# Kernel tuning notes

Measured on AMD Instinct MI355X. Metric: run time of the kernel, lower is better.

The kernel has to match this reference:

```python
import jax, jax.numpy as jnp
import numpy as np
from functools import partial

# FCOSPostProcessor config (from __init__ defaults / hard-coded forward constants)
PRE_NMS_THRESH = 0.05
PRE_NMS_TOP_N = 1000
ML_NMS_THRESH = 0.6       # self.nms_thresh used in select_over_all_levels
FPN_POST_NMS_TOP_N = 100
SCORE_THRESH = 0.5        # hard-coded in forward
FINAL_NMS_THRESH = 0.9    # hard-coded in forward
NUM_CLASSES = 17          # 16 foreground logit channels

_STRIDES = (8, 16, 32, 64, 128)
_FEAT_HW = ((100, 160), (50, 80), (25, 40), (13, 20), (7, 10))
_BATCH = 8
_C = NUM_CLASSES - 1


def setup_inputs() -> dict:
    key = jax.random.key(0)
    inp = {}
    for lvl, (s, (h, w)) in enumerate(zip(_STRIDES, _FEAT_HW)):
        k1, k2, k3 = jax.random.split(jax.random.fold_in(key, lvl), 3)
        ys = jnp.arange(h, dtype=jnp.float32) * s + s // 2
        xs = jnp.arange(w, dtype=jnp.float32) * s + s // 2
        yy, xx = jnp.meshgrid(ys, xs, indexing='ij')
        inp[f'locations_{lvl}'] = jnp.stack([xx.reshape(-1), yy.reshape(-1)], axis=-1)  # (h*w, 2) xy
        inp[f'box_cls_{lvl}'] = jax.random.normal(k1, (_BATCH, _C, h, w), jnp.float32) * 2.0 - 5.0
        inp[f'box_regression_{lvl}'] = jax.random.uniform(k2, (_BATCH, 4, h, w), jnp.float32) * (4.0 * s)
        inp[f'centerness_{lvl}'] = jax.random.normal(k3, (_BATCH, 1, h, w), jnp.float32)
    inp['image_sizes'] = jnp.tile(jnp.array([[800, 1280]], jnp.int32), (_BATCH, 1))  # (h, w)
    return inp


def _decode_level(loc, cls, reg, ctr, image_sizes):
    # cls: (N,C,H,W) -> (N,HW,C) sigmoid; reg: (N,4,H,W) -> (N,HW,4); ctr: (N,1,H,W) -> (N,HW)
    N, C, H, W = cls.shape
    cls_s = jax.nn.sigmoid(jnp.transpose(cls, (0, 2, 3, 1)).reshape(N, H * W, C))
    reg_r = jnp.transpose(reg, (0, 2, 3, 1)).reshape(N, H * W, 4)
    ctr_s = jax.nn.sigmoid(ctr.reshape(N, H * W))
    cand = (cls_s > PRE_NMS_THRESH).reshape(N, -1)          # candidate mask (N, HW*C)
    sc = (cls_s * ctr_s[:, :, None]).reshape(N, -1)         # cls * centerness
    masked = jnp.where(cand, sc, -1.0)
    top_s, top_i = jax.lax.top_k(masked, PRE_NMS_TOP_N)     # padded top-k over threshold survivors
    valid = jnp.take_along_axis(cand, top_i, axis=1)
    loc_i = top_i // C
    labels = (top_i % C + 1).astype(jnp.int32)              # per_class = idx + 1
    pl = loc[loc_i]                                         # (N,K,2)
    idx4 = jnp.broadcast_to(loc_i[:, :, None], loc_i.shape + (4,))
    pr = jnp.take_along_axis(reg_r, idx4, axis=1)           # (N,K,4)
    x1 = pl[..., 0] - pr[..., 0]
    y1 = pl[..., 1] - pr[..., 1]
    x2 = pl[..., 0] + pr[..., 2]
    y2 = pl[..., 1] + pr[..., 3]
    # clip_to_image (TO_REMOVE = 1)
    hmax = (image_sizes[:, 0] - 1).astype(x1.dtype)[:, None]
    wmax = (image_sizes[:, 1] - 1).astype(x1.dtype)[:, None]
    boxes = jnp.stack([jnp.clip(x1, 0.0, wmax), jnp.clip(y1, 0.0, hmax),
                       jnp.clip(x2, 0.0, wmax), jnp.clip(y2, 0.0, hmax)], axis=-1)
    scores = jnp.where(valid, jnp.sqrt(jnp.maximum(top_s, 1e-12)), 0.0)  # sqrt(cls*ctr)
    return boxes, scores, labels, valid


def _iou(a, b):
    area_a = jnp.maximum(a[:, 2] - a[:, 0], 0.0) * jnp.maximum(a[:, 3] - a[:, 1], 0.0)
    area_b = jnp.maximum(b[:, 2] - b[:, 0], 0.0) * jnp.maximum(b[:, 3] - b[:, 1], 0.0)
    lt = jnp.maximum(a[:, None, :2], b[None, :, :2])
    rb = jnp.minimum(a[:, None, 2:], b[None, :, 2:])
    wh = jnp.maximum(rb - lt, 0.0)
    inter = wh[..., 0] * wh[..., 1]
    return inter / jnp.maximum(area_a[:, None] + area_b[None, :] - inter, 1e-9)


def _greedy_keep(boxes, scores, valid, thresh):
    # fixed-size greedy NMS on a single image; selection is discrete -> stop_gradient
    boxes = jax.lax.stop_gradient(boxes)
    scores = jax.lax.stop_gradient(scores)
    K = scores.shape[0]
    order = jnp.argsort(-jnp.where(valid, scores, -1.0))
    b = boxes[order]
    v = valid[order]
    iou = _iou(b, b)
    idx = jnp.arange(K)
    def body(i, keep):
        sup = (iou[i] > thresh) & keep[i] & (idx > i)
        return keep & (~sup)
    keep = jax.lax.fori_loop(0, K, body, v)
    return jnp.zeros(K, bool).at[order].set(keep)


def _pipeline(locs, clss, regs, ctrs, image_sizes):
    parts = [_decode_level(l, c, r, t, image_sizes)
             for l, c, r, t in zip(locs, clss, regs, ctrs)]
    boxes = jnp.concatenate([p[0] for p in parts], axis=1)   # (N, 5K, 4)
    scores = jnp.concatenate([p[1] for p in parts], axis=1)
    labels = jnp.concatenate([p[2] for p in parts], axis=1)
    valid = jnp.concatenate([p[3] for p in parts], axis=1)
    # multi-class NMS (boxlist_ml_nms): offset boxes per class so classes never overlap
    off = labels.astype(boxes.dtype) * (jax.lax.stop_gradient(jnp.max(boxes)) + 1.0)
    keep = jax.vmap(partial(_greedy_keep, thresh=ML_NMS_THRESH))(boxes + off[..., None], scores, valid)
    valid = valid & keep
    # fpn_post_nms_top_n cap (kthvalue-threshold in torch ~= top-k by score)
    _, idx = jax.lax.top_k(jnp.where(valid, scores, -1.0), FPN_POST_NMS_TOP_N)
    boxes = jnp.take_along_axis(boxes, jnp.broadcast_to(idx[:, :, None], idx.shape + (4,)), axis=1)
    scores = jnp.take_along_axis(scores, idx, axis=1)
    labels = jnp.take_along_axis(labels, idx, axis=1)
    valid = jnp.take_along_axis(valid, idx, axis=1)
    # choose_confident_boxes(score_thresh=0.5)
    valid = valid & (scores > SCORE_THRESH)
    # final class-agnostic boxlist_nms(0.9)
    keep2 = jax.vmap(partial(_greedy_keep, thresh=FINAL_NMS_THRESH))(boxes, scores, valid)
    valid = valid & keep2
    return (jnp.where(valid[..., None], boxes, 0.0),
            jnp.where(valid, scores, 0.0),
            jnp.where(valid, labels, 0),
            valid)


def reference(locations_0, locations_1, locations_2, locations_3, locations_4,
              box_cls_0, box_cls_1, box_cls_2, box_cls_3, box_cls_4,
              box_regression_0, box_regression_1, box_regression_2, box_regression_3, box_regression_4,
              centerness_0, centerness_1, centerness_2, centerness_3, centerness_4,
              image_sizes):
    locs = (locations_0, locations_1, locations_2, locations_3, locations_4)
    clss = (box_cls_0, box_cls_1, box_cls_2, box_cls_3, box_cls_4)
    regs = (box_regression_0, box_regression_1, box_regression_2, box_regression_3, box_regression_4)
    ctrs = (centerness_0, centerness_1, centerness_2, centerness_3, centerness_4)
    return _pipeline(locs, clss, regs, ctrs, image_sizes)
```

## Files before the change

kernel.cpp:

```cpp
#include <hip/hip_runtime.h>

#pragma clang fp contract(off)

typedef unsigned int u32;
typedef unsigned long long u64;
typedef unsigned char u8;

#define NIMG 8
#define NCLS 16
#define KSEL 1000
#define KIMG 5000
#define TOPN 100
#define CAP 576
#define NWRD 9
#define TIECAP 128
#define EPI 341280
#define HCH 4096
#define HBLK 84
#define ECH 16384
#define EBLK 23

__device__ inline int lvl_of(int i) {
  return (i < 256000) ? 0 : (i < 320000) ? 1 : (i < 336000) ? 2 : (i < 340160) ? 3 : 4;
}
__device__ inline int c_hw(int l)   { return l==0?16000: l==1?4000: l==2?1000: l==3?260: 70; }
__device__ inline int c_eoff(int l) { return l==0?0: l==1?256000: l==2?320000: l==3?336000: l==4?340160: 341280; }
__device__ inline int c_e(int l)    { return l==0?256000: l==1?64000: l==2?16000: l==3?4160: 1120; }

__device__ inline void blk_map(int b, int& lvl, int& bb, int& start, int& end) {
  if (b < 16)      { lvl = 0; bb = b; }
  else if (b < 20) { lvl = 1; bb = b - 16; }
  else             { lvl = b - 18; bb = 0; }
  start = c_eoff(lvl) + bb*ECH;
  int e = c_eoff(lvl + 1);
  end = (start + ECH < e) ? (start + ECH) : e;
}

struct Ptrs {
  const float* loc[5];
  const float* cls[5];
  const float* reg[5];
  const float* ctr[5];
  const int*   imsz;
};

__device__ inline u64 lmask_lt(int lane) { return lane ? (~0ull >> (64 - lane)) : 0ull; }

__device__ inline float sigm(float x) { return 1.0f / (1.0f + expf(-x)); }

__device__ inline float score_cand(const Ptrs& P, int img, int lvl, int c, int hw, bool& cand) {
  int HW = c_hw(lvl);
  float s = sigm(P.cls[lvl][(img*NCLS + c)*HW + hw]);
  cand = s > 0.05f;
  float t = sigm(P.ctr[lvl][img*HW + hw]);
  return s * t;
}

__device__ inline void box_decode(const Ptrs& P, int img, int lvl, int hw,
                                  float& x1, float& y1, float& x2, float& y2) {
  int HW = c_hw(lvl);
  float px = P.loc[lvl][hw*2+0];
  float py = P.loc[lvl][hw*2+1];
  float rl = P.reg[lvl][(img*4+0)*HW + hw];
  float rt = P.reg[lvl][(img*4+1)*HW + hw];
  float rr = P.reg[lvl][(img*4+2)*HW + hw];
  float rb = P.reg[lvl][(img*4+3)*HW + hw];
  float wmax = (float)(P.imsz[img*2+1] - 1);
  float hmax = (float)(P.imsz[img*2+0] - 1);
  x1 = fminf(fmaxf(px - rl, 0.0f), wmax);
  y1 = fminf(fmaxf(py - rt, 0.0f), hmax);
  x2 = fminf(fmaxf(px + rr, 0.0f), wmax);
  y2 = fminf(fmaxf(py + rb, 0.0f), hmax);
}

struct Det { float x1, y1, x2, y2, raw; bool cand; };

__device__ inline Det decode(const Ptrs& P, int img, int lvl, int c, int hw) {
  Det d;
  d.raw = score_cand(P, img, lvl, c, hw, d.cand);
  box_decode(P, img, lvl, hw, d.x1, d.y1, d.x2, d.y2);
  return d;
}

__device__ inline float iou_ref(float ax1, float ay1, float ax2, float ay2,
                                float bx1, float by1, float bx2, float by2) {
  float areaA = fmaxf(ax2-ax1, 0.0f) * fmaxf(ay2-ay1, 0.0f);
  float areaB = fmaxf(bx2-bx1, 0.0f) * fmaxf(by2-by1, 0.0f);
  float wx = fmaxf(fminf(ax2,bx2) - fmaxf(ax1,bx1), 0.0f);
  float wy = fmaxf(fminf(ay2,by2) - fmaxf(ay1,by1), 0.0f);
  float inter = wx * wy;
  return inter / fmaxf(areaA + areaB - inter, 1e-9f);
}

__global__ void k_zero(u32* w, int n) {
  for (int i = blockIdx.x*blockDim.x + threadIdx.x; i < n; i += gridDim.x*blockDim.x) {
    u32 val = 0;
    int rel = i - 40960;
    if (rel >= 0 && rel < 320 && (rel & 7) == 2) val = KSEL;
    w[i] = val;
  }
}

__global__ __launch_bounds__(256) void k_hist(Ptrs P, u32* hist, const u32* state, int pass) {
  __shared__ u32 lh[2][1024];
  int img = blockIdx.y;
  int chunk = blockIdx.x * HCH;
  for (int b = threadIdx.x; b < 2048; b += 256) ((u32*)lh)[b] = 0;
  int lvl0 = lvl_of(chunk);
  int prob0 = img*5 + lvl0;
  bool straddle = (lvl0 < 4) && (chunk + HCH > c_eoff(lvl0+1));
  u32 m0 = state[prob0*8+0], p0 = state[prob0*8+1];
  u32 m1 = 0, p1 = 0;
  if (straddle) { m1 = state[(prob0+1)*8+0]; p1 = state[(prob0+1)*8+1]; }
  int shift = (pass == 0) ? 20 : ((pass == 1) ? 10 : 0);
  __syncthreads();
  for (int k = 0; k < 16; ++k) {
    int i = chunk + k*256 + threadIdx.x;
    if (i >= EPI) break;
    int lvl = lvl0 + ((straddle && i >= c_eoff(lvl0+1)) ? 1 : 0);
    int li = i - c_eoff(lvl);
    int HW = c_hw(lvl);
    int c = li / HW, hw = li - c*HW;
    bool cand; float raw = score_cand(P, img, lvl, c, hw, cand);
    if (!cand) continue;
    u32 bits = __float_as_uint(raw);
    int bank = lvl - lvl0;
    u32 msk = bank ? m1 : m0, pfx = bank ? p1 : p0;
    if ((bits & msk) != pfx) continue;
    atomicAdd(&lh[bank][(bits >> shift) & 0x3FFu], 1u);
  }
  __syncthreads();
  for (int b = threadIdx.x; b < 2048; b += 256) {
    u32 v = ((u32*)lh)[b];
    if (v) atomicAdd(&hist[(prob0 + (b >> 10))*1024 + (b & 1023)], v);
  }
}

__global__ __launch_bounds__(256) void k_scan(u32* hist, u32* state, int pass) {
  __shared__ u32 sfx[1024];
  __shared__ int sbin;
  int prob = blockIdx.x;
  u32* h = hist + prob*1024;
  int tid = threadIdx.x;
  for (int r = tid; r < 1024; r += 256) sfx[r] = h[1023 - r];
  __syncthreads();
  for (int b = tid; b < 1024; b += 256) h[b] = 0;
  if (tid == 0) sbin = -1;
  for (int d = 1; d < 1024; d <<= 1) {
    u32 v[4];
#pragma unroll
    for (int k = 0; k < 4; ++k) {
      int i = tid + k*256;
      v[k] = sfx[i] + ((i >= d) ? sfx[i - d] : 0u);
    }
    __syncthreads();
#pragma unroll
    for (int k = 0; k < 4; ++k) sfx[tid + k*256] = v[k];
    __syncthreads();
  }
  u32 need = state[prob*8+2];
  u32 allM = state[prob*8+3];
  if (!allM) {
#pragma unroll
    for (int k = 0; k < 4; ++k) {
      int b = tid + k*256;
      u32 sb  = sfx[1023 - b];
      u32 sb1 = (b == 1023) ? 0u : sfx[1022 - b];
      if (sb >= need && sb1 < need) sbin = b;
    }
  }
  __syncthreads();
  if (tid == 0 && !allM) {
    u32* st = state + prob*8;
    if (sbin < 0) {
      st[3] = 1; st[0] = 0xFFFFFFFFu; st[1] = 0xFFFFFFFFu;
    } else {
      int shift = (pass == 0) ? 20 : ((pass == 1) ? 10 : 0);
      u32 rem = need - ((sbin == 1023) ? 0u : sfx[1022 - sbin]);
      st[1] |= ((u32)sbin) << shift;
      st[0] |= 0x3FFu << shift;
      st[2] = rem;
      if (pass == 2) { st[4] = st[1]; st[5] = rem; }
    }
  }
}

__global__ __launch_bounds__(256) void k_count(Ptrs P, const u32* state, u32* blockCnt) {
  int lvl, bb, start, end;
  blk_map(blockIdx.x, lvl, bb, start, end);
  int img = blockIdx.y;
  int prob = img*5 + lvl;
  int HW = c_hw(lvl);
  const float* clsBase = P.cls[lvl] + (size_t)img*NCLS*HW;
  const float* ctrBase = P.ctr[lvl] + (size_t)img*HW;
  u32 allMode = state[prob*8+3];
  u32 tstar = state[prob*8+4];
  int cnt = 0;
  for (int r = 0; r < 16; ++r) {
    int i0 = start + r*1024 + threadIdx.x*4;
    if (i0 >= end) continue;
    int li = i0 - c_eoff(lvl);
    float4 cv;
    if (i0 + 4 <= end) cv = *reinterpret_cast<const float4*>(clsBase + li);
    else {
      cv.x = clsBase[li];
      cv.y = (i0+1 < end) ? clsBase[li+1] : 0.0f;
      cv.z = (i0+2 < end) ? clsBase[li+2] : 0.0f;
      cv.w = (i0+3 < end) ? clsBase[li+3] : 0.0f;
    }
#pragma unroll
    for (int e = 0; e < 4; ++e) {
      int i = i0 + e;
      if (i >= end) break;
      float s = sigm((&cv.x)[e]);
      if (!(s > 0.05f)) continue;
      int lie = li + e;
      int hw = lie % HW;
      float t = sigm(ctrBase[hw]);
      u32 bits = __float_as_uint(s * t);
      if (allMode || bits > tstar) ++cnt;
    }
  }
  for (int d = 32; d >= 1; d >>= 1) cnt += __shfl_xor(cnt, d);
  __shared__ int ws[4];
  if ((threadIdx.x & 63) == 0) ws[threadIdx.x >> 6] = cnt;
  __syncthreads();
  if (threadIdx.x == 0) blockCnt[prob*16 + bb] = (u32)(ws[0] + ws[1] + ws[2] + ws[3]);
}

__global__ void k_bscan(const u32* blockCnt, u32* bbase, u32* counter) {
  int p = threadIdx.x;
  if (p >= 40) return;
  int lvl = p % 5;
  int nb = (lvl == 0) ? 16 : (lvl == 1) ? 4 : 1;
  u32 run = 0;
  for (int b = 0; b < nb; ++b) { bbase[p*16 + b] = run; run += blockCnt[p*16 + b]; }
  counter[p] = run;
}

__global__ __launch_bounds__(256) void k_emit(Ptrs P, const u32* state, const u32* bbase,
                                              u32* tieCnt, u32* tieIdx,
                                              u32* sbits, float* ssqrt, u32* slabel,
                                              float* sbox, u32* gmax) {
  __shared__ u32 wcnt[2][4];
  int lvl, bb, start, end;
  blk_map(blockIdx.x, lvl, bb, start, end);
  int img = blockIdx.y;
  int prob = img*5 + lvl;
  int HW = c_hw(lvl);
  const float* clsBase = P.cls[lvl] + (size_t)img*NCLS*HW;
  const float* ctrBase = P.ctr[lvl] + (size_t)img*HW;
  u32 allMode = state[prob*8+3];
  u32 tstar = state[prob*8+4];
  int lane = threadIdx.x & 63, wv = threadIdx.x >> 6;
  u64 lt = lmask_lt(lane);
  int running = (int)bbase[prob*16 + bb];
  float wmax = 0.0f;
  for (int r = 0; r < 16; ++r) {
    int i0 = start + r*1024 + threadIdx.x*4;
    int li = i0 - c_eoff(lvl);
    bool w[4] = {false,false,false,false};
    u32 bits[4] = {0,0,0,0};
    if (i0 < end) {
      float4 cv;
      if (i0 + 4 <= end) cv = *reinterpret_cast<const float4*>(clsBase + li);
      else {
        cv.x = clsBase[li];
        cv.y = (i0+1 < end) ? clsBase[li+1] : 0.0f;
        cv.z = (i0+2 < end) ? clsBase[li+2] : 0.0f;
        cv.w = (i0+3 < end) ? clsBase[li+3] : 0.0f;
      }
#pragma unroll
      for (int e = 0; e < 4; ++e) {
        int i = i0 + e;
        if (i >= end) break;
        float s = sigm((&cv.x)[e]);
        if (!(s > 0.05f)) continue;
        int lie = li + e;
        int c = lie / HW, hw = lie - c*HW;
        float t = sigm(ctrBase[hw]);
        u32 bi = __float_as_uint(s * t);
        if (allMode || bi > tstar) { w[e] = true; bits[e] = bi; }
        else if (bi == tstar) {
          u32 ts = atomicAdd(&tieCnt[prob], 1u);
          if (ts < TIECAP) tieIdx[prob*TIECAP + ts] = (u32)(hw*NCLS + c);
        }
      }
    }
    u64 b0 = __ballot(w[0]), b1 = __ballot(w[1]), b2 = __ballot(w[2]), b3 = __ballot(w[3]);
    int wvTot = (int)(__popcll(b0) + __popcll(b1) + __popcll(b2) + __popcll(b3));
    if (lane == 0) wcnt[r & 1][wv] = (u32)wvTot;
    __syncthreads();
    int preWave = 0, blockTot = 0;
#pragma unroll
    for (int k = 0; k < 4; ++k) {
      int v = (int)wcnt[r & 1][k];
      if (k < wv) preWave += v;
      blockTot += v;
    }
    int before = (int)(__popcll(b0 & lt) + __popcll(b1 & lt) + __popcll(b2 & lt) + __popcll(b3 & lt));
    int myBase = running + preWave + before;
    int acc = 0;
#pragma unroll
    for (int e = 0; e < 4; ++e) {
      if (!w[e]) continue;
      int slot = myBase + acc; ++acc;
      if (slot < KSEL) {
        int lie = li + e;
        int c = lie / HW, hw = lie - c*HW;
        float raw = __uint_as_float(bits[e]);
        float x1, y1, x2, y2;
        box_decode(P, img, lvl, hw, x1, y1, x2, y2);
        int idx = img*KIMG + lvl*KSEL + slot;
        sbits[idx]  = bits[e];
        ssqrt[idx]  = sqrtf(fmaxf(raw, 1e-12f));
        slabel[idx] = (u32)(c + 1);
        sbox[idx*4+0] = x1; sbox[idx*4+1] = y1;
        sbox[idx*4+2] = x2; sbox[idx*4+3] = y2;
        wmax = fmaxf(wmax, fmaxf(fmaxf(x1, y1), fmaxf(x2, y2)));
      }
    }
    running += blockTot;
  }
  for (int d = 32; d >= 1; d >>= 1) wmax = fmaxf(wmax, __shfl_xor(wmax, d));
  if (lane == 0 && wmax > 0.0f) atomicMax(gmax, __float_as_uint(wmax));
}

__global__ void k_ties(Ptrs P, const u32* state, u32* counter, const u32* tieCnt, const u32* tieIdx,
                       u32* sbits, float* ssqrt, u32* slabel, float* sbox, u32* gmax) {
  __shared__ u32 a[TIECAP];
  int prob = blockIdx.x;
  const u32* st = state + prob*8;
  if (st[3]) return;
  if (threadIdx.x != 0) return;
  int tn = (tieCnt[prob] < (u32)TIECAP) ? (int)tieCnt[prob] : TIECAP;
  int need = (int)st[5];
  int take = need < tn ? need : tn;
  if (take <= 0) return;
  for (int k = 0; k < tn; ++k) a[k] = tieIdx[prob*TIECAP + k];
  for (int k = 1; k < tn; ++k) {
    u32 v = a[k]; int m = k - 1;
    while (m >= 0 && a[m] > v) { a[m+1] = a[m]; --m; }
    a[m+1] = v;
  }
  int img = prob/5, lvl = prob%5;
  u32 cnt = counter[prob];
  for (int k = 0; k < take && cnt < (u32)KSEL; ++k) {
    u32 e = a[k]; int hw = (int)(e >> 4), c = (int)(e & 15u);
    Det d = decode(P, img, lvl, c, hw);
    int idx = img*KIMG + lvl*KSEL + (int)cnt;
    sbits[idx]  = __float_as_uint(d.raw);
    ssqrt[idx]  = sqrtf(fmaxf(d.raw, 1e-12f));
    slabel[idx] = (u32)(c + 1);
    sbox[idx*4+0] = d.x1; sbox[idx*4+1] = d.y1;
    sbox[idx*4+2] = d.x2; sbox[idx*4+3] = d.y2;
    float m4 = fmaxf(fmaxf(d.x1, d.y1), fmaxf(d.x2, d.y2));
    atomicMax(gmax, __float_as_uint(m4));
    ++cnt;
  }
  counter[prob] = cnt;
}

__global__ void k_deficit(Ptrs P, const u32* counter, u32* gmax) {
  int prob = blockIdx.x;
  int cnt = (int)counter[prob];
  if (cnt >= KSEL) return;
  int deficit = KSEL - cnt;
  int img = prob/5, lvl = prob%5;
  int E = c_e(lvl);
  int HW = c_hw(lvl);
  const float* clsBase = P.cls[lvl] + (size_t)img*NCLS*HW;
  int lane = threadIdx.x;
  int found = 0;
  float wmax = 0.0f;
  for (int base = 0; base < E && found < deficit; base += 64) {
    int e = base + lane;
    bool nc = false;
    if (e < E) nc = !(sigm(clsBase[(e & 15)*HW + (e >> 4)]) > 0.05f);
    u64 m = __ballot(nc);
    int pos = found + (int)__popcll(m & lmask_lt(lane));
    if (nc && pos < deficit) {
      float x1, y1, x2, y2;
      box_decode(P, img, lvl, e >> 4, x1, y1, x2, y2);
      wmax = fmaxf(wmax, fmaxf(fmaxf(x1, y1), fmaxf(x2, y2)));
    }
    found += (int)__popcll(m);
  }
  for (int d = 32; d >= 1; d >>= 1) wmax = fmaxf(wmax, __shfl_xor(wmax, d));
  if (lane == 0 && wmax > 0.0f) atomicMax(gmax, __float_as_uint(wmax));
}

__global__ __launch_bounds__(1024) void k_sort(const u32* sbits, u64* skey) {
  __shared__ u64 sk[8192];
  int img = blockIdx.x;
  int tid = threadIdx.x, nth = blockDim.x;
  for (int i = tid; i < 8192; i += nth)
    sk[i] = (i < KIMG) ? ((((u64)sbits[img*KIMG + i]) << 32) | (u32)(KIMG - 1 - i)) : 0ull;
  __syncthreads();
  for (int ksz = 2; ksz <= 8192; ksz <<= 1) {
    for (int j = ksz >> 1; j >= 1; j >>= 1) {
      for (int i = tid; i < 8192; i += nth) {
        int ixj = i ^ j;
        if (ixj > i) {
          bool desc = ((i & ksz) == 0);
          u64 a = sk[i], b = sk[ixj];
          if (desc ? (a < b) : (a > b)) { sk[i] = b; sk[ixj] = a; }
        }
      }
      __syncthreads();
    }
  }
  for (int i = tid; i < KIMG; i += nth) skey[img*KIMG + i] = sk[i];
}

__device__ inline int key_slot(u64 key) { return KIMG - 1 - (int)(key & 0xFFFFFFFFu); }

__global__ __launch_bounds__(256) void k_nms(const u64* skey, const u32* slabel, const float* sbox,
                                             const u32* gmax, u8* keep) {
  __shared__ float4 sb[CAP];
  __shared__ u32 srank[CAP];
  __shared__ u64 bm[CAP][NWRD];
  __shared__ u32 wcnt[4];
  __shared__ u64 kw[NWRD];
  __shared__ int sn;
  int img = blockIdx.x >> 4;
  int cls = (blockIdx.x & 15) + 1;
  int tid = threadIdx.x;
  int lane = tid & 63;
  int wv = tid >> 6;
  float off = (float)cls * (__uint_as_float(*gmax) + 1.0f);
  if (tid == 0) sn = 0;
  __syncthreads();
  for (int base = 0; base < KIMG; base += 256) {
    int r = base + tid;
    bool v = false; int slot = 0;
    if (r < KIMG) {
      u64 key = skey[img*KIMG + r];
      slot = key_slot(key);
      if ((key >> 32) != 0) v = (slabel[img*KIMG + slot] == (u32)cls);
    }
    u64 m = __ballot(v);
    int wrank = (int)__popcll(m & lmask_lt(lane));
    if (lane == 0) wcnt[wv] = (u32)__popcll(m);
    __syncthreads();
    int pos = sn + wrank;
    for (int k = 0; k < 4; ++k) if (k < wv) pos += (int)wcnt[k];
    if (v && pos < CAP) {
      const float* b = &sbox[(img*KIMG + slot)*4];
      sb[pos] = make_float4(b[0]+off, b[1]+off, b[2]+off, b[3]+off);
      srank[pos] = (u32)r;
    }
    __syncthreads();
    if (tid == 0) sn += (int)(wcnt[0]+wcnt[1]+wcnt[2]+wcnt[3]);
    __syncthreads();
  }
  int n = sn; if (n > CAP) n = CAP;
  for (int i = tid; i < n; i += 256) {
    float4 bi = sb[i];
    u64 w[NWRD];
#pragma unroll
    for (int q = 0; q < NWRD; ++q) w[q] = 0;
    for (int j = i + 1; j < n; ++j) {
      float4 bj = sb[j];
      if (iou_ref(bj.x,bj.y,bj.z,bj.w, bi.x,bi.y,bi.z,bi.w) > 0.6f)
        w[j >> 6] |= (1ull << (j & 63));
    }
#pragma unroll
    for (int q = 0; q < NWRD; ++q) bm[i][q] = w[q];
  }
  __syncthreads();
  if (wv == 0) {
    u64 kp = 0;
    if (lane < NWRD) {
      int cnt = n - lane*64;
      kp = (cnt >= 64) ? ~0ull : (cnt > 0 ? ((1ull << cnt) - 1ull) : 0ull);
    }
    for (int i = 0; i < n; ++i) {
      u64 row = (lane < NWRD) ? bm[i][lane] : 0ull;
      u64 kow = __shfl(kp, i >> 6);
      if ((kow >> (i & 63)) & 1ull) kp &= ~row;
    }
    if (lane < NWRD) kw[lane] = kp;
  }
  __syncthreads();
  for (int j = tid; j < n; j += 256)
    keep[img*KIMG + (int)srank[j]] = (u8)((kw[j >> 6] >> (j & 63)) & 1ull);
}

__global__ __launch_bounds__(64) void k_final(const u64* skey, const u8* keep, const float* ssqrt,
                                              const u32* slabel, const float* sbox, float* out) {
  __shared__ float sc[TOPN];
  __shared__ u32 lb[TOPN];
  __shared__ float4 bx[TOPN];
  int img = blockIdx.x;
  int lane = threadIdx.x;
  int cnt = 0;
  for (int base = 0; base < KIMG && cnt < TOPN; base += 64) {
    int r = base + lane;
    bool v = false; int slot = 0;
    if (r < KIMG) {
      u64 key = skey[img*KIMG + r];
      slot = key_slot(key);
      v = ((key >> 32) != 0) && (keep[img*KIMG + r] != 0);
    }
    u64 m = __ballot(v);
    int pos = cnt + (int)__popcll(m & lmask_lt(lane));
    if (v && pos < TOPN) {
      int sidx = img*KIMG + slot;
      sc[pos] = ssqrt[sidx];
      lb[pos] = slabel[sidx];
      bx[pos] = make_float4(sbox[sidx*4+0], sbox[sidx*4+1], sbox[sidx*4+2], sbox[sidx*4+3]);
    }
    cnt += (int)__popcll(m);
  }
  int n2 = cnt < TOPN ? cnt : TOPN;
  __syncthreads();
  u32 sup = 0;
  for (int i = 0; i < n2; ++i) {
    int owner = i & 63, s = i >> 6;
    u32 om = __shfl(sup, owner);
    bool vi = sc[i] > 0.5f;
    if (!vi || ((om >> s) & 1u)) continue;
    float4 bi = bx[i];
#pragma unroll
    for (int k = 0; k < 2; ++k) {
      int j = lane + (k << 6);
      if (j > i && j < n2 && !((sup >> k) & 1u)) {
        float4 bj = bx[j];
        if (iou_ref(bj.x, bj.y, bj.z, bj.w, bi.x, bi.y, bi.z, bi.w) > 0.9f)
          sup |= (1u << k);
      }
    }
  }
#pragma unroll
  for (int k = 0; k < 2; ++k) {
    int j = lane + (k << 6);
    if (j < TOPN) {
      bool ok = (j < n2) && (sc[j] > 0.5f) && !((sup >> k) & 1u);
      float4 b = ok ? bx[j] : make_float4(0.f, 0.f, 0.f, 0.f);
      float s  = ok ? sc[j] : 0.0f;
      float lf = ok ? (float)lb[j] : 0.0f;
      float vf = ok ? 1.0f : 0.0f;
      int ob = img*TOPN + j;
      out[ob*4+0] = b.x; out[ob*4+1] = b.y; out[ob*4+2] = b.z; out[ob*4+3] = b.w;
      out[NIMG*TOPN*4 + ob] = s;
      out[NIMG*TOPN*5 + ob] = lf;
      out[NIMG*TOPN*6 + ob] = vf;
    }
  }
}

extern "C" void kernel_launch(void* const* d_in, const int* in_sizes, int n_in,
                              void* d_out, int out_size, void* d_ws, size_t ws_size,
                              hipStream_t stream) {
  Ptrs P;
  bool dictOrder = (n_in >= 21) && (in_sizes[1] == 2048000);
  if (dictOrder) {
    for (int l = 0; l < 5; ++l) {
      P.loc[l] = (const float*)d_in[4*l + 0];
      P.cls[l] = (const float*)d_in[4*l + 1];
      P.reg[l] = (const float*)d_in[4*l + 2];
      P.ctr[l] = (const float*)d_in[4*l + 3];
    }
    P.imsz = (const int*)d_in[20];
  } else {
    for (int l = 0; l < 5; ++l) {
      P.loc[l] = (const float*)d_in[l];
      P.cls[l] = (const float*)d_in[5 + l];
      P.reg[l] = (const float*)d_in[10 + l];
      P.ctr[l] = (const float*)d_in[15 + l];
    }
    P.imsz = (const int*)d_in[20];
  }

  char* w = (char*)d_ws;
  u32* hist    = (u32*)w;  w += 40*1024*4;
  u32* state   = (u32*)w;  w += 40*8*4;
  u32* tieCnt  = (u32*)w;  w += 40*4;
  u32* gmax    = (u32*)w;  w += 64;
  u32* sbits   = (u32*)w;  w += NIMG*KIMG*4;
  u8*  keep    = (u8*)w;   w += NIMG*KIMG;
  size_t zbytes = (size_t)(w - (char*)d_ws);
  u32* counter  = (u32*)w;  w += 40*4;
  u32* blockCnt = (u32*)w;  w += 40*16*4;
  u32* bbase    = (u32*)w;  w += 40*16*4;
  u32* tieIdx   = (u32*)w;  w += 40*TIECAP*4;
  float* ssqrt  = (float*)w; w += NIMG*KIMG*4;
  u32* slabel   = (u32*)w;  w += NIMG*KIMG*4;
  float* sbox   = (float*)w; w += NIMG*KIMG*16;
  u64* skey     = (u64*)w;  w += NIMG*KIMG*8;

  size_t used = (size_t)(w - (char*)d_ws);
  if (used > ws_size) return;
  int zwords = (int)(zbytes / 4);

  k_zero<<<96, 256, 0, stream>>>((u32*)d_ws, zwords);
  for (int pass = 0; pass < 3; ++pass) {
    k_hist<<<dim3(HBLK, NIMG), 256, 0, stream>>>(P, hist, state, pass);
    k_scan<<<40, 256, 0, stream>>>(hist, state, pass);
  }
  k_count<<<dim3(EBLK, NIMG), 256, 0, stream>>>(P, state, blockCnt);
  k_bscan<<<1, 64, 0, stream>>>(blockCnt, bbase, counter);
  k_emit<<<dim3(EBLK, NIMG), 256, 0, stream>>>(P, state, bbase, tieCnt, tieIdx,
                                               sbits, ssqrt, slabel, sbox, gmax);
  k_ties<<<40, 64, 0, stream>>>(P, state, counter, tieCnt, tieIdx,
                                sbits, ssqrt, slabel, sbox, gmax);
  k_deficit<<<40, 64, 0, stream>>>(P, counter, gmax);
  k_sort<<<NIMG, 1024, 0, stream>>>(sbits, skey);
  k_nms<<<NIMG*NCLS, 256, 0, stream>>>(skey, slabel, sbox, gmax, keep);
  k_final<<<NIMG, 64, 0, stream>>>(skey, keep, ssqrt, slabel, sbox, (float*)d_out);
}
```

Before: 541.0 us.

## Split per-image bitonic sort into per-level sorts plus rank-based merge

Replaces the single 8192-element bitonic sort per image (8 blocks) with 40 blocks that each sort one level's 1000 candidates, followed by a merge kernel that places each key by binary-search ranking against the other four sorted lists. This spreads the sort across more blocks and cuts the bitonic stage count and padding work. It adds a kernel launch and an extra global buffer, and changes the slot encoding in the key's low bits so that keys stay unique and nonzero.

```diff
diff --git a/kernel.cpp b/kernel.cpp
--- a/kernel.cpp
+++ b/kernel.cpp
@@ -390,16 +390,23 @@
   if (lane == 0 && wmax > 0.0f) atomicMax(gmax, __float_as_uint(wmax));
 }
 
-__global__ __launch_bounds__(1024) void k_sort(const u32* sbits, u64* skey) {
-  __shared__ u64 sk[8192];
-  int img = blockIdx.x;
-  int tid = threadIdx.x, nth = blockDim.x;
-  for (int i = tid; i < 8192; i += nth)
-    sk[i] = (i < KIMG) ? ((((u64)sbits[img*KIMG + i]) << 32) | (u32)(KIMG - 1 - i)) : 0ull;
-  __syncthreads();
-  for (int ksz = 2; ksz <= 8192; ksz <<= 1) {
+__global__ __launch_bounds__(512) void k_sortlvl(const u32* sbits, u64* lkey) {
+  __shared__ u64 sk[1024];
+  int prob = blockIdx.x;
+  int img = prob/5, lvl = prob%5;
+  int tid = threadIdx.x;
+  for (int i = tid; i < 1024; i += 512) {
+    u64 key = 0ull;
+    if (i < KSEL) {
+      int slot = lvl*KSEL + i;
+      key = (((u64)sbits[img*KIMG + slot]) << 32) | (u32)(KIMG - slot);
+    }
+    sk[i] = key;
+  }
+  __syncthreads();
+  for (int ksz = 2; ksz <= 1024; ksz <<= 1) {
     for (int j = ksz >> 1; j >= 1; j >>= 1) {
-      for (int i = tid; i < 8192; i += nth) {
+      for (int i = tid; i < 1024; i += 512) {
         int ixj = i ^ j;
         if (ixj > i) {
           bool desc = ((i & ksz) == 0);
@@ -410,10 +417,35 @@
       __syncthreads();
     }
   }
-  for (int i = tid; i < KIMG; i += nth) skey[img*KIMG + i] = sk[i];
-}
-
-__device__ inline int key_slot(u64 key) { return KIMG - 1 - (int)(key & 0xFFFFFFFFu); }
+  for (int i = tid; i < KSEL; i += 512) lkey[prob*KSEL + i] = sk[i];
+}
+
+__global__ __launch_bounds__(256) void k_merge(const u64* lkey, u64* skey) {
+  __shared__ u64 ll[5][KSEL];
+  int prob = blockIdx.x;
+  int img = prob/5, lvl = prob%5;
+  int tid = threadIdx.x;
+  for (int i = tid; i < 5*KSEL; i += 256)
+    ll[i/KSEL][i%KSEL] = lkey[img*KIMG + i];
+  __syncthreads();
+  for (int j = tid; j < KSEL; j += 256) {
+    u64 key = ll[lvl][j];
+    int rank = j;
+#pragma unroll
+    for (int l2 = 0; l2 < 5; ++l2) {
+      if (l2 == lvl) continue;
+      int lo = 0, hi = KSEL;
+      while (lo < hi) {
+        int mid = (lo + hi) >> 1;
+        if (ll[l2][mid] > key) lo = mid + 1; else hi = mid;
+      }
+      rank += lo;
+    }
+    skey[img*KIMG + rank] = key;
+  }
+}
+
+__device__ inline int key_slot(u64 key) { return KIMG - (int)(key & 0xFFFFFFFFu); }
 
 __global__ __launch_bounds__(256) void k_nms(const u64* skey, const u32* slabel, const float* sbox,
                                              const u32* gmax, u8* keep) {
@@ -589,6 +621,7 @@
   u32* slabel   = (u32*)w;  w += NIMG*KIMG*4;
   float* sbox   = (float*)w; w += NIMG*KIMG*16;
   u64* skey     = (u64*)w;  w += NIMG*KIMG*8;
+  u64* lkey     = (u64*)w;  w += NIMG*KIMG*8;
 
   size_t used = (size_t)(w - (char*)d_ws);
   if (used > ws_size) return;
@@ -606,7 +639,8 @@
   k_ties<<<40, 64, 0, stream>>>(P, state, counter, tieCnt, tieIdx,
                                 sbits, ssqrt, slabel, sbox, gmax);
   k_deficit<<<40, 64, 0, stream>>>(P, counter, gmax);
-  k_sort<<<NIMG, 1024, 0, stream>>>(sbits, skey);
+  k_sortlvl<<<40, 512, 0, stream>>>(sbits, lkey);
+  k_merge<<<40, 256, 0, stream>>>(lkey, skey);
   k_nms<<<NIMG*NCLS, 256, 0, stream>>>(skey, slabel, sbox, gmax, keep);
   k_final<<<NIMG, 64, 0, stream>>>(skey, keep, ssqrt, slabel, sbox, (float*)d_out);
 }
```

Measured after the change: 459.5 us. 15.1% less time.
